# Kernel tuning notes

Hardware: AMD Instinct MI355X
Metric: run time of the kernel (lower is better)

Reference implementation:

```python
import jax, jax.numpy as jnp
import numpy as np

B, CAP, H, NH = 128, 65536, 512, 8
HD = H // NH
GH = H // 4  # gate hidden


def setup_inputs() -> dict:
    key = jax.random.key(0)
    ks = jax.random.split(key, 8)
    s = 1.0 / np.sqrt(H)
    sg = 1.0 / np.sqrt(GH)
    return {
        "query": jax.random.normal(ks[0], (B, H), jnp.float32),
        "memory_keys": jax.random.normal(ks[1], (CAP, H), jnp.float32) * s,
        "memory_values": jax.random.normal(ks[2], (CAP, H), jnp.float32) * s,
        "in_proj_w": jax.random.normal(ks[3], (3 * H, H), jnp.float32) * s,
        "in_proj_b": jnp.zeros((3 * H,), jnp.float32),
        "out_proj_w": jax.random.normal(ks[4], (H, H), jnp.float32) * s,
        "out_proj_b": jnp.zeros((H,), jnp.float32),
        "gate_w1": jax.random.normal(ks[5], (GH, H), jnp.float32) * s,
        "gate_b1": jnp.zeros((GH,), jnp.float32),
        "gate_w2": jax.random.normal(ks[6], (1, GH), jnp.float32) * sg,
        "gate_b2": jnp.zeros((1,), jnp.float32),
        "usage_count": jnp.zeros((CAP,), jnp.float32),
        "last_used": jnp.zeros((CAP,), jnp.float32),
        "step_counter": 1,
    }


def reference(query, memory_keys, memory_values, in_proj_w, in_proj_b,
              out_proj_w, out_proj_b, gate_w1, gate_b1, gate_w2, gate_b2,
              usage_count, last_used, step_counter):
    # nn.MultiheadAttention packed projections: rows [0:H]=Wq, [H:2H]=Wk, [2H:3H]=Wv
    wq, wk, wv = in_proj_w[:H], in_proj_w[H:2 * H], in_proj_w[2 * H:]
    bq, bk, bv = in_proj_b[:H], in_proj_b[H:2 * H], in_proj_b[2 * H:]

    q = (query @ wq.T + bq).reshape(B, NH, HD)           # [B, h, d] (q_len = 1)
    k = (memory_keys @ wk.T + bk).reshape(CAP, NH, HD)   # [C, h, d]
    v = (memory_values @ wv.T + bv).reshape(CAP, NH, HD)  # [C, h, d]

    scores = jnp.einsum('bhd,chd->bhc', q, k) / np.sqrt(HD)  # [B, h, C]
    attn = jax.nn.softmax(scores, axis=-1)
    ctx = jnp.einsum('bhc,chd->bhd', attn, v).reshape(B, H)
    attn_out = ctx @ out_proj_w.T + out_proj_b               # [B, H]

    # usage bookkeeping: attn_weights averaged over heads, then over batch
    avg_attn = attn.mean(axis=(0, 1))                        # [C]
    new_usage = usage_count + avg_attn
    new_last = jnp.where(avg_attn > 1e-3,
                         jnp.float32(step_counter), last_used)

    # gating MLP: Linear -> ReLU -> Linear -> Sigmoid
    gate = jax.nn.sigmoid(
        jax.nn.relu(query @ gate_w1.T + gate_b1) @ gate_w2.T + gate_b2)  # [B, 1]
    memory_output = gate * attn_out                          # [B, H]
    return memory_output, new_usage, new_last
```

## Files before the change

### kernel.cpp

```cpp
#include <hip/hip_runtime.h>
#include <stdint.h>


typedef __bf16 b16x8 __attribute__((ext_vector_type(8)));
typedef float f32x4 __attribute__((ext_vector_type(4)));

static __device__ __forceinline__ unsigned short f2bf(float f) {
  return __builtin_bit_cast(unsigned short, (__bf16)f);
}

static __device__ __forceinline__ f32x4 MFMA(b16x8 a, b16x8 b, f32x4 c) {
  return __builtin_amdgcn_mfma_f32_16x16x32_bf16(a, b, c, 0, 0, 0);
}

#define GLL16(g, l)                                                          \
  __builtin_amdgcn_global_load_lds(                                          \
      (const __attribute__((address_space(1))) void*)(g),                    \
      (__attribute__((address_space(3))) void*)(l), 16, 0, 0)

__global__ void k_convert_w(const float* __restrict__ w, unsigned short* __restrict__ dst) {
  int i = blockIdx.x * 256 + threadIdx.x;
  float4 v = reinterpret_cast<const float4*>(w + 512 * 512)[i];
  ushort4 o;
  o.x = f2bf(v.x); o.y = f2bf(v.y); o.z = f2bf(v.z); o.w = f2bf(v.w);
  reinterpret_cast<ushort4*>(dst)[i] = o;
}

__global__ void k_proj_q(const float* __restrict__ query, const float* __restrict__ w,
                         const float* __restrict__ bias, unsigned short* __restrict__ qout) {
  __shared__ float qs[512];
  int b = blockIdx.x, j = threadIdx.x;
  qs[j] = query[b * 512 + j];
  __syncthreads();
  float acc = bias[j];
  const float4* q4 = reinterpret_cast<const float4*>(qs);
  const float4* w4 = reinterpret_cast<const float4*>(w + j * 512);
#pragma unroll 8
  for (int i = 0; i < 128; ++i) {
    float4 a = q4[i], c = w4[i];
    acc += a.x * c.x + a.y * c.y + a.z * c.z + a.w * c.w;
  }
  qout[b * 512 + j] = f2bf(acc);
}

__global__ void k_gate(const float* __restrict__ query, const float* __restrict__ w1,
                       const float* __restrict__ b1, const float* __restrict__ w2,
                       const float* __restrict__ b2, float* __restrict__ gate) {
  __shared__ float qs[512];
  __shared__ float red[2];
  int b = blockIdx.x, j = threadIdx.x;
  qs[j] = query[b * 512 + j];
  qs[j + 128] = query[b * 512 + j + 128];
  qs[j + 256] = query[b * 512 + j + 256];
  qs[j + 384] = query[b * 512 + j + 384];
  __syncthreads();
  float acc = b1[j];
  const float4* q4 = reinterpret_cast<const float4*>(qs);
  const float4* w4 = reinterpret_cast<const float4*>(w1 + j * 512);
#pragma unroll 8
  for (int i = 0; i < 128; ++i) {
    float4 a = q4[i], c = w4[i];
    acc += a.x * c.x + a.y * c.y + a.z * c.z + a.w * c.w;
  }
  float t = fmaxf(acc, 0.f) * w2[j];
#pragma unroll
  for (int off = 1; off < 64; off <<= 1) t += __shfl_xor(t, off, 64);
  if ((j & 63) == 0) red[j >> 6] = t;
  __syncthreads();
  if (j == 0) {
    float z = red[0] + red[1] + b2[0];
    gate[b] = 1.f / (1.f + __builtin_amdgcn_exp2f(-z * 1.44269504088896f));
  }
}

__global__ __launch_bounds__(512, 4) void k_proj_kv(
    const float* __restrict__ mk, const float* __restrict__ mv,
    const unsigned short* __restrict__ wkb, const unsigned short* __restrict__ wvb,
    const float* __restrict__ in_b,
    unsigned short* __restrict__ kout, unsigned short* __restrict__ vtout) {
  const int p = blockIdx.x;
  const int xcd = p & 7, slot = p >> 3;
  const int isV = xcd >> 2;
  const int j0 = (slot & 3) * 128;
  const int c0 = (xcd & 3) * 16384 + (slot >> 2) * 128;
  const float* Ag = isV ? mv : mk;
  const unsigned short* W = isV ? wvb : wkb;
  const float* bias = in_b + (isV ? 1024 : 512);
  const int tid = threadIdx.x;
  const int w = tid >> 6, wr = w >> 2, wc = w & 3;
  const int ln = tid & 15, g = (tid & 63) >> 4;
  const int sw = (ln >> 1) & 3;

  __shared__ __align__(16) unsigned short Al[2][128 * 32];
  __shared__ __align__(16) unsigned short Wl[2][128 * 32];

  f32x4 acc[4][2];
#pragma unroll
  for (int m = 0; m < 4; ++m)
#pragma unroll
    for (int n = 0; n < 2; ++n) acc[m][n] = {0.f, 0.f, 0.f, 0.f};

  const int arow = tid >> 2, aq = tid & 3;
  const float* aptr = Ag + (size_t)(c0 + arow) * 512 + aq * 8;
  const int aoff = arow * 32 + ((aq ^ ((arow >> 1) & 3)) << 3);

  const int lane = tid & 63;
  const int wrow = 16 * w + (lane >> 2);
  const int wps = (lane & 3) ^ ((wrow >> 1) & 3);
  const unsigned short* wsrc = W + (size_t)(j0 + wrow) * 512 + wps * 8;
  const int wdoff = w * 512;

  float4 aA0, aA1, aB0, aB1;
  {
    GLL16(wsrc, &Wl[0][wdoff]);
    const float4* ap = reinterpret_cast<const float4*>(aptr);
    aA0 = ap[0]; aA1 = ap[1];
    b16x8 v;
    v[0] = (__bf16)aA0.x; v[1] = (__bf16)aA0.y; v[2] = (__bf16)aA0.z; v[3] = (__bf16)aA0.w;
    v[4] = (__bf16)aA1.x; v[5] = (__bf16)aA1.y; v[6] = (__bf16)aA1.z; v[7] = (__bf16)aA1.w;
    *reinterpret_cast<b16x8*>(&Al[0][aoff]) = v;
    const float4* ap1 = reinterpret_cast<const float4*>(aptr + 32);
    aB0 = ap1[0]; aB1 = ap1[1];
  }
  __syncthreads();

#pragma unroll 2
  for (int kk = 0; kk < 16; ++kk) {
    const int cur = kk & 1, nxt = cur ^ 1;
    if (kk < 14) {
      const float4* ap = reinterpret_cast<const float4*>(aptr + (kk + 2) * 32);
      if (cur == 0) { aA0 = ap[0]; aA1 = ap[1]; }
      else          { aB0 = ap[0]; aB1 = ap[1]; }
    }
    if (kk < 15) GLL16(wsrc + (kk + 1) * 32, &Wl[nxt][wdoff]);

    b16x8 af[4], wf[2];
#pragma unroll
    for (int m = 0; m < 4; ++m) {
      int row = 64 * wr + 16 * m + ln;
      af[m] = *reinterpret_cast<const b16x8*>(&Al[cur][row * 32 + ((g ^ sw) << 3)]);
    }
#pragma unroll
    for (int n = 0; n < 2; ++n) {
      int row = 32 * wc + 16 * n + ln;
      wf[n] = *reinterpret_cast<const b16x8*>(&Wl[cur][row * 32 + ((g ^ sw) << 3)]);
    }
    if (!isV) {
#pragma unroll
      for (int m = 0; m < 4; ++m)
#pragma unroll
        for (int n = 0; n < 2; ++n) acc[m][n] = MFMA(wf[n], af[m], acc[m][n]);
    } else {
#pragma unroll
      for (int m = 0; m < 4; ++m)
#pragma unroll
        for (int n = 0; n < 2; ++n) acc[m][n] = MFMA(af[m], wf[n], acc[m][n]);
    }
    if (kk < 15) {
      float4 f0 = (nxt == 0) ? aA0 : aB0, f1 = (nxt == 0) ? aA1 : aB1;
      b16x8 v;
      v[0] = (__bf16)f0.x; v[1] = (__bf16)f0.y; v[2] = (__bf16)f0.z; v[3] = (__bf16)f0.w;
      v[4] = (__bf16)f1.x; v[5] = (__bf16)f1.y; v[6] = (__bf16)f1.z; v[7] = (__bf16)f1.w;
      *reinterpret_cast<b16x8*>(&Al[nxt][aoff]) = v;
    }
    __syncthreads();
  }

  if (!isV) {
#pragma unroll
    for (int m = 0; m < 4; ++m) {
      int c = c0 + 64 * wr + 16 * m + ln;
#pragma unroll
      for (int n = 0; n < 2; ++n) {
        int jb = j0 + 32 * wc + 16 * n + 4 * g;
        float4 bb = *reinterpret_cast<const float4*>(&bias[jb]);
        ushort4 o;
        o.x = f2bf(acc[m][n][0] + bb.x);
        o.y = f2bf(acc[m][n][1] + bb.y);
        o.z = f2bf(acc[m][n][2] + bb.z);
        o.w = f2bf(acc[m][n][3] + bb.w);
        *reinterpret_cast<ushort4*>(&kout[(size_t)c * 512 + jb]) = o;
      }
    }
  } else {
#pragma unroll
    for (int n = 0; n < 2; ++n) {
      int j = j0 + 32 * wc + 16 * n + ln;
      float bj = bias[j];
#pragma unroll
      for (int m = 0; m < 4; ++m) {
        int cb = c0 + 64 * wr + 16 * m + 4 * g;
        ushort4 o;
        o.x = f2bf(acc[m][n][0] + bj);
        o.y = f2bf(acc[m][n][1] + bj);
        o.z = f2bf(acc[m][n][2] + bj);
        o.w = f2bf(acc[m][n][3] + bj);
        *reinterpret_cast<ushort4*>(&vtout[(size_t)j * 65536 + cb]) = o;
      }
    }
  }
}

__global__ __launch_bounds__(256) void k_attn1(
    const unsigned short* __restrict__ kb, const unsigned short* __restrict__ vt,
    const unsigned short* __restrict__ qb,
    float* __restrict__ l_ws, float* __restrict__ ctxT) {
  const int h = blockIdx.y, cg = blockIdx.x;
  const int tid = threadIdx.x;
  const int wv = tid >> 6, wr = wv >> 1, wc = wv & 1;
  const int ln = tid & 15, g = (tid & 63) >> 4;
  __shared__ __align__(16) unsigned short kS[128 * 64];
  __shared__ __align__(16) unsigned short pS[128 * 128];
  __shared__ __align__(16) unsigned short vS[64 * 128];
  const float SC = 0.125f * 1.44269504088896f;

  b16x8 qf[4][2];
#pragma unroll
  for (int n = 0; n < 4; ++n)
#pragma unroll
    for (int ks = 0; ks < 2; ++ks) {
      int b = 64 * wc + 16 * n + ln;
      qf[n][ks] = *reinterpret_cast<const b16x8*>(&qb[(size_t)b * 512 + h * 64 + ks * 32 + g * 8]);
    }
  f32x4 pacc[2][4];
#pragma unroll
  for (int m = 0; m < 2; ++m)
#pragma unroll
    for (int n = 0; n < 4; ++n) pacc[m][n] = {0.f, 0.f, 0.f, 0.f};
  float lsum[4] = {0.f, 0.f, 0.f, 0.f};

  for (int it = 0; it < 8; ++it) {
    int c0g = cg * 1024 + it * 128;
#pragma unroll
    for (int i = 0; i < 4; ++i) {
      int fl = i * 256 + tid, row = fl >> 3, p8 = fl & 7;
      uint4 d = *reinterpret_cast<const uint4*>(&kb[(size_t)(c0g + row) * 512 + h * 64 + p8 * 8]);
      *reinterpret_cast<uint4*>(&kS[(row * 8 + (p8 ^ (row & 7))) * 8]) = d;
    }
#pragma unroll
    for (int i = 0; i < 4; ++i) {
      int fl = i * 256 + tid, row = fl >> 4, p16 = fl & 15;
      uint4 d = *reinterpret_cast<const uint4*>(&vt[(size_t)(h * 64 + row) * 65536 + c0g + p16 * 8]);
      *reinterpret_cast<uint4*>(&vS[(row * 16 + (p16 ^ (row & 7))) * 8]) = d;
    }
    __syncthreads();

    f32x4 sacc[4][4];
#pragma unroll
    for (int m = 0; m < 4; ++m)
#pragma unroll
      for (int n = 0; n < 4; ++n) sacc[m][n] = {0.f, 0.f, 0.f, 0.f};
#pragma unroll
    for (int ks = 0; ks < 2; ++ks) {
      b16x8 a[4];
#pragma unroll
      for (int m = 0; m < 4; ++m) {
        int row = 64 * wr + 16 * m + ln;
        a[m] = *reinterpret_cast<const b16x8*>(&kS[(row * 8 + ((ks * 4 + g) ^ (row & 7))) * 8]);
      }
#pragma unroll
      for (int m = 0; m < 4; ++m)
#pragma unroll
        for (int n = 0; n < 4; ++n) sacc[m][n] = MFMA(a[m], qf[n][ks], sacc[m][n]);
    }
#pragma unroll
    for (int m = 0; m < 4; ++m)
#pragma unroll
      for (int n = 0; n < 4; ++n) {
        float p0 = __builtin_amdgcn_exp2f(sacc[m][n][0] * SC);
        float p1 = __builtin_amdgcn_exp2f(sacc[m][n][1] * SC);
        float p2 = __builtin_amdgcn_exp2f(sacc[m][n][2] * SC);
        float p3 = __builtin_amdgcn_exp2f(sacc[m][n][3] * SC);
        lsum[n] += (p0 + p1) + (p2 + p3);
        int b = 64 * wc + 16 * n + ln;
        int c = 64 * wr + 16 * m + 4 * g;
        int base = b * 128 + (((c >> 3) ^ (b & 7)) * 8) + (c & 7);
        ushort2 lo, hi;
        lo.x = f2bf(p0); lo.y = f2bf(p1);
        hi.x = f2bf(p2); hi.y = f2bf(p3);
        *reinterpret_cast<ushort2*>(&pS[base]) = lo;
        *reinterpret_cast<ushort2*>(&pS[base + 2]) = hi;
      }
    __syncthreads();
#pragma unroll
    for (int ks = 0; ks < 4; ++ks) {
      b16x8 av[2], bp[4];
#pragma unroll
      for (int m = 0; m < 2; ++m) {
        int row = 32 * wr + 16 * m + ln;
        av[m] = *reinterpret_cast<const b16x8*>(&vS[(row * 16 + ((ks * 4 + g) ^ (row & 7))) * 8]);
      }
#pragma unroll
      for (int n = 0; n < 4; ++n) {
        int row = 64 * wc + 16 * n + ln;
        bp[n] = *reinterpret_cast<const b16x8*>(&pS[(row * 16 + ((ks * 4 + g) ^ (row & 7))) * 8]);
      }
#pragma unroll
      for (int m = 0; m < 2; ++m)
#pragma unroll
        for (int n = 0; n < 4; ++n) pacc[m][n] = MFMA(av[m], bp[n], pacc[m][n]);
    }
    __syncthreads();
  }
#pragma unroll
  for (int n = 0; n < 4; ++n) {
    float v = lsum[n];
    v += __shfl_xor(v, 16, 64);
    v += __shfl_xor(v, 32, 64);
    if ((tid & 63) < 16) atomicAdd(&l_ws[h * 128 + 64 * wc + 16 * n + ln], v);
  }
#pragma unroll
  for (int m = 0; m < 2; ++m)
#pragma unroll
    for (int n = 0; n < 4; ++n)
#pragma unroll
      for (int r = 0; r < 4; ++r) {
        int d = 32 * wr + 16 * m + 4 * g + r;
        int b = 64 * wc + 16 * n + ln;
        atomicAdd(&ctxT[(h * 64 + d) * 128 + b], pacc[m][n][r]);
      }
}

__global__ __launch_bounds__(256) void k_attn2(
    const unsigned short* __restrict__ kb, const unsigned short* __restrict__ qb,
    const float* __restrict__ l_ws, float* __restrict__ avgA) {
  const int h = blockIdx.y, cg = blockIdx.x;
  const int tid = threadIdx.x;
  const int wv = tid >> 6, wr = wv >> 1, wc = wv & 1;
  const int ln = tid & 15, g = (tid & 63) >> 4;
  __shared__ __align__(16) unsigned short kS[128 * 64];
  __shared__ float wS[128];
  const float SC = 0.125f * 1.44269504088896f;
  if (tid < 128) wS[tid] = 1.f / l_ws[h * 128 + tid];
  b16x8 qf[4][2];
#pragma unroll
  for (int n = 0; n < 4; ++n)
#pragma unroll
    for (int ks = 0; ks < 2; ++ks) {
      int b = 64 * wc + 16 * n + ln;
      qf[n][ks] = *reinterpret_cast<const b16x8*>(&qb[(size_t)b * 512 + h * 64 + ks * 32 + g * 8]);
    }
  __syncthreads();
  float wn[4];
#pragma unroll
  for (int n = 0; n < 4; ++n) wn[n] = wS[64 * wc + 16 * n + ln];

  for (int it = 0; it < 8; ++it) {
    int c0g = cg * 1024 + it * 128;
#pragma unroll
    for (int i = 0; i < 4; ++i) {
      int fl = i * 256 + tid, row = fl >> 3, p8 = fl & 7;
      uint4 d = *reinterpret_cast<const uint4*>(&kb[(size_t)(c0g + row) * 512 + h * 64 + p8 * 8]);
      *reinterpret_cast<uint4*>(&kS[(row * 8 + (p8 ^ (row & 7))) * 8]) = d;
    }
    __syncthreads();
    f32x4 sacc[4][4];
#pragma unroll
    for (int m = 0; m < 4; ++m)
#pragma unroll
      for (int n = 0; n < 4; ++n) sacc[m][n] = {0.f, 0.f, 0.f, 0.f};
#pragma unroll
    for (int ks = 0; ks < 2; ++ks) {
      b16x8 a[4];
#pragma unroll
      for (int m = 0; m < 4; ++m) {
        int row = 64 * wr + 16 * m + ln;
        a[m] = *reinterpret_cast<const b16x8*>(&kS[(row * 8 + ((ks * 4 + g) ^ (row & 7))) * 8]);
      }
#pragma unroll
      for (int m = 0; m < 4; ++m)
#pragma unroll
        for (int n = 0; n < 4; ++n) sacc[m][n] = MFMA(a[m], qf[n][ks], sacc[m][n]);
    }
#pragma unroll
    for (int m = 0; m < 4; ++m) {
      float s0 = 0.f, s1 = 0.f, s2 = 0.f, s3 = 0.f;
#pragma unroll
      for (int n = 0; n < 4; ++n) {
        s0 += __builtin_amdgcn_exp2f(sacc[m][n][0] * SC) * wn[n];
        s1 += __builtin_amdgcn_exp2f(sacc[m][n][1] * SC) * wn[n];
        s2 += __builtin_amdgcn_exp2f(sacc[m][n][2] * SC) * wn[n];
        s3 += __builtin_amdgcn_exp2f(sacc[m][n][3] * SC) * wn[n];
      }
#pragma unroll
      for (int off = 1; off < 16; off <<= 1) {
        s0 += __shfl_xor(s0, off, 64);
        s1 += __shfl_xor(s1, off, 64);
        s2 += __shfl_xor(s2, off, 64);
        s3 += __shfl_xor(s3, off, 64);
      }
      if (ln == 0) {
        int c = c0g + 64 * wr + 16 * m + 4 * g;
        atomicAdd(&avgA[c], s0);
        atomicAdd(&avgA[c + 1], s1);
        atomicAdd(&avgA[c + 2], s2);
        atomicAdd(&avgA[c + 3], s3);
      }
    }
    __syncthreads();
  }
}

__global__ void k_finalize(const float* __restrict__ ctxT, const float* __restrict__ l_ws,
                           const float* __restrict__ wout, const float* __restrict__ bout,
                           const float* __restrict__ gate, float* __restrict__ out) {
  __shared__ float cs[512];
  int b = blockIdx.x, j = threadIdx.x;
  cs[j] = ctxT[j * 128 + b] / l_ws[(j >> 6) * 128 + b];
  __syncthreads();
  float acc = bout[j];
  const float4* c4 = reinterpret_cast<const float4*>(cs);
  const float4* w4 = reinterpret_cast<const float4*>(wout + j * 512);
#pragma unroll 8
  for (int i = 0; i < 128; ++i) {
    float4 a = c4[i], c = w4[i];
    acc += a.x * c.x + a.y * c.y + a.z * c.z + a.w * c.w;
  }
  out[b * 512 + j] = gate[b] * acc;
}

__global__ void k_usage(const float* __restrict__ avgA, const float* __restrict__ usage,
                        const float* __restrict__ last, const int* __restrict__ step,
                        float* __restrict__ out_usage, float* __restrict__ out_last) {
  int c = blockIdx.x * 256 + threadIdx.x;
  float avg = avgA[c] * (1.f / 1024.f);
  out_usage[c] = usage[c] + avg;
  out_last[c] = (avg > 0.001f) ? (float)step[0] : last[c];
}

extern "C" void kernel_launch(void* const* d_in, const int* in_sizes, int n_in,
                              void* d_out, int out_size, void* d_ws, size_t ws_size,
                              hipStream_t stream) {
  const float* query = (const float*)d_in[0];
  const float* mk    = (const float*)d_in[1];
  const float* mv    = (const float*)d_in[2];
  const float* in_w  = (const float*)d_in[3];
  const float* in_b  = (const float*)d_in[4];
  const float* out_w = (const float*)d_in[5];
  const float* out_b = (const float*)d_in[6];
  const float* gw1   = (const float*)d_in[7];
  const float* gb1   = (const float*)d_in[8];
  const float* gw2   = (const float*)d_in[9];
  const float* gb2   = (const float*)d_in[10];
  const float* usage = (const float*)d_in[11];
  const float* last  = (const float*)d_in[12];
  const int*   step  = (const int*)d_in[13];

  char* ws = (char*)d_ws;
  unsigned short* qb  = (unsigned short*)(ws);
  unsigned short* wkb = (unsigned short*)(ws + 131072);
  unsigned short* wvb = (unsigned short*)(ws + 655360);
  unsigned short* kb  = (unsigned short*)(ws + 1179648);
  unsigned short* vt  = (unsigned short*)(ws + 68288512);
  float* l_ws = (float*)(ws + 135397376);
  float* ctxT = (float*)(ws + 135401472);
  float* avgA = (float*)(ws + 135663616);
  float* gate = (float*)(ws + 135925760);
  float* out = (float*)d_out;

  hipMemsetAsync(ws + 135397376, 0, 4096 + 262144 + 262144, stream);

  k_convert_w<<<512, 256, 0, stream>>>(in_w, wkb);
  k_proj_q<<<128, 512, 0, stream>>>(query, in_w, in_b, qb);
  k_gate<<<128, 128, 0, stream>>>(query, gw1, gb1, gw2, gb2, gate);
  k_proj_kv<<<4096, 512, 0, stream>>>(mk, mv, wkb, wvb, in_b, kb, vt);
  k_attn1<<<dim3(64, 8), 256, 0, stream>>>(kb, vt, qb, l_ws, ctxT);
  k_attn2<<<dim3(64, 8), 256, 0, stream>>>(kb, qb, l_ws, avgA);
  k_finalize<<<128, 512, 0, stream>>>(ctxT, l_ws, out_w, out_b, gate, out);
  k_usage<<<256, 256, 0, stream>>>(avgA, usage, last, step, out + 65536, out + 131072);
}
```

Baseline: 371.7 us.

## Stage full 128-row A tile in LDS once and loop over all output column tiles

The K/V projection kernel now converts a whole 128x512 block of memory keys/values to bf16 into LDS once (128 KB, XOR-swizzled), then iterates over all four 128-column output tiles. Each fp32 input row is read from global memory once instead of four times. Weight tiles stream through a 4-slot LDS ring via global_load_lds, with explicit vmcnt waits and sched barriers in place of full __syncthreads. The grid shrinks to 1024 blocks and launch bounds drop to 2 blocks per CU, trading occupancy and load/compute overlap during the A staging phase for less global traffic.

After: 345.7 us. 1.08x faster.

```diff
diff --git a/kernel.cpp b/kernel.cpp
--- a/kernel.cpp
+++ b/kernel.cpp
@@ -17,6 +17,8 @@
   __builtin_amdgcn_global_load_lds(                                          \
       (const __attribute__((address_space(1))) void*)(g),                    \
       (__attribute__((address_space(3))) void*)(l), 16, 0, 0)
+
+#define SBAR() __builtin_amdgcn_sched_barrier(0)
 
 __global__ void k_convert_w(const float* __restrict__ w, unsigned short* __restrict__ dst) {
   int i = blockIdx.x * 256 + threadIdx.x;
@@ -73,132 +75,127 @@
   }
 }
 
-__global__ __launch_bounds__(512, 4) void k_proj_kv(
+__global__ __launch_bounds__(512, 2) void k_proj_kv(
     const float* __restrict__ mk, const float* __restrict__ mv,
     const unsigned short* __restrict__ wkb, const unsigned short* __restrict__ wvb,
     const float* __restrict__ in_b,
     unsigned short* __restrict__ kout, unsigned short* __restrict__ vtout) {
   const int p = blockIdx.x;
-  const int xcd = p & 7, slot = p >> 3;
-  const int isV = xcd >> 2;
-  const int j0 = (slot & 3) * 128;
-  const int c0 = (xcd & 3) * 16384 + (slot >> 2) * 128;
+  const int isV = p & 1;
+  const int c0 = (p >> 1) * 128;
   const float* Ag = isV ? mv : mk;
   const unsigned short* W = isV ? wvb : wkb;
   const float* bias = in_b + (isV ? 1024 : 512);
   const int tid = threadIdx.x;
-  const int w = tid >> 6, wr = w >> 2, wc = w & 3;
+  const int w = tid >> 6, lane = tid & 63;
+  const int wr = w >> 2, wc = w & 3;
   const int ln = tid & 15, g = (tid & 63) >> 4;
-  const int sw = (ln >> 1) & 3;
-
-  __shared__ __align__(16) unsigned short Al[2][128 * 32];
-  __shared__ __align__(16) unsigned short Wl[2][128 * 32];
-
-  f32x4 acc[4][2];
-#pragma unroll
-  for (int m = 0; m < 4; ++m)
-#pragma unroll
-    for (int n = 0; n < 2; ++n) acc[m][n] = {0.f, 0.f, 0.f, 0.f};
-
-  const int arow = tid >> 2, aq = tid & 3;
-  const float* aptr = Ag + (size_t)(c0 + arow) * 512 + aq * 8;
-  const int aoff = arow * 32 + ((aq ^ ((arow >> 1) & 3)) << 3);
-
-  const int lane = tid & 63;
+
+  __shared__ __align__(16) unsigned short AL[65536];
+  __shared__ __align__(16) unsigned short WL[4][4096];
+
   const int wrow = 16 * w + (lane >> 2);
-  const int wps = (lane & 3) ^ ((wrow >> 1) & 3);
-  const unsigned short* wsrc = W + (size_t)(j0 + wrow) * 512 + wps * 8;
-  const int wdoff = w * 512;
-
-  float4 aA0, aA1, aB0, aB1;
-  {
-    GLL16(wsrc, &Wl[0][wdoff]);
-    const float4* ap = reinterpret_cast<const float4*>(aptr);
-    aA0 = ap[0]; aA1 = ap[1];
+  const int wcs = (lane & 3) ^ ((wrow >> 1) & 3);
+  const unsigned short* wsrc = W + (size_t)wrow * 512 + wcs * 8;
+  const int wdst = w * 512;
+
+  GLL16(wsrc, &WL[0][wdst]);
+  GLL16(wsrc + 32, &WL[1][wdst]);
+
+#pragma unroll 4
+  for (int c = 0; c < 16; ++c) {
+    int row = c * 8 + w;
+    const float* src = Ag + (size_t)(c0 + row) * 512 + lane * 8;
+    float4 f0 = *reinterpret_cast<const float4*>(src);
+    float4 f1 = *reinterpret_cast<const float4*>(src + 4);
     b16x8 v;
-    v[0] = (__bf16)aA0.x; v[1] = (__bf16)aA0.y; v[2] = (__bf16)aA0.z; v[3] = (__bf16)aA0.w;
-    v[4] = (__bf16)aA1.x; v[5] = (__bf16)aA1.y; v[6] = (__bf16)aA1.z; v[7] = (__bf16)aA1.w;
-    *reinterpret_cast<b16x8*>(&Al[0][aoff]) = v;
-    const float4* ap1 = reinterpret_cast<const float4*>(aptr + 32);
-    aB0 = ap1[0]; aB1 = ap1[1];
-  }
-  __syncthreads();
-
-#pragma unroll 2
-  for (int kk = 0; kk < 16; ++kk) {
-    const int cur = kk & 1, nxt = cur ^ 1;
-    if (kk < 14) {
-      const float4* ap = reinterpret_cast<const float4*>(aptr + (kk + 2) * 32);
-      if (cur == 0) { aA0 = ap[0]; aA1 = ap[1]; }
-      else          { aB0 = ap[0]; aB1 = ap[1]; }
-    }
-    if (kk < 15) GLL16(wsrc + (kk + 1) * 32, &Wl[nxt][wdoff]);
-
-    b16x8 af[4], wf[2];
-#pragma unroll
-    for (int m = 0; m < 4; ++m) {
-      int row = 64 * wr + 16 * m + ln;
-      af[m] = *reinterpret_cast<const b16x8*>(&Al[cur][row * 32 + ((g ^ sw) << 3)]);
-    }
-#pragma unroll
-    for (int n = 0; n < 2; ++n) {
-      int row = 32 * wc + 16 * n + ln;
-      wf[n] = *reinterpret_cast<const b16x8*>(&Wl[cur][row * 32 + ((g ^ sw) << 3)]);
-    }
+    v[0] = (__bf16)f0.x; v[1] = (__bf16)f0.y; v[2] = (__bf16)f0.z; v[3] = (__bf16)f0.w;
+    v[4] = (__bf16)f1.x; v[5] = (__bf16)f1.y; v[6] = (__bf16)f1.z; v[7] = (__bf16)f1.w;
+    int chunk = lane ^ (row & 7);
+    *reinterpret_cast<b16x8*>(&AL[row * 512 + chunk * 8]) = v;
+  }
+  __syncthreads();
+
+#pragma unroll
+  for (int jt = 0; jt < 4; ++jt) {
+    const int j0 = jt * 128;
+    f32x4 acc[4][2];
+#pragma unroll
+    for (int m = 0; m < 4; ++m)
+#pragma unroll
+      for (int n = 0; n < 2; ++n) acc[m][n] = {0.f, 0.f, 0.f, 0.f};
+
+#pragma unroll
+    for (int kk = 0; kk < 16; ++kk) {
+      const int t = jt * 16 + kk;
+      const int tn = (t + 2 <= 63) ? t + 2 : 63;
+      const int slot = (t + 2) & 3;
+      GLL16(wsrc + (size_t)(tn >> 4) * 65536 + (tn & 15) * 32, &WL[slot][wdst]);
+      SBAR();
+      asm volatile("s_waitcnt vmcnt(2)" ::: "memory");
+      SBAR();
+      __builtin_amdgcn_s_barrier();
+      SBAR();
+      b16x8 af[4], wf[2];
+#pragma unroll
+      for (int m = 0; m < 4; ++m) {
+        int r = 64 * wr + 16 * m + ln;
+        int ch = (kk * 4 + g) ^ (r & 7);
+        af[m] = *reinterpret_cast<const b16x8*>(&AL[r * 512 + ch * 8]);
+      }
+#pragma unroll
+      for (int n = 0; n < 2; ++n) {
+        int r = 32 * wc + 16 * n + ln;
+        wf[n] = *reinterpret_cast<const b16x8*>(&WL[t & 3][r * 32 + ((g ^ ((r >> 1) & 3)) << 3)]);
+      }
+      if (!isV) {
+#pragma unroll
+        for (int m = 0; m < 4; ++m)
+#pragma unroll
+          for (int n = 0; n < 2; ++n) acc[m][n] = MFMA(wf[n], af[m], acc[m][n]);
+      } else {
+#pragma unroll
+        for (int m = 0; m < 4; ++m)
+#pragma unroll
+          for (int n = 0; n < 2; ++n) acc[m][n] = MFMA(af[m], wf[n], acc[m][n]);
+      }
+    }
+
     if (!isV) {
 #pragma unroll
-      for (int m = 0; m < 4; ++m)
-#pragma unroll
-        for (int n = 0; n < 2; ++n) acc[m][n] = MFMA(wf[n], af[m], acc[m][n]);
+      for (int m = 0; m < 4; ++m) {
+        int c = c0 + 64 * wr + 16 * m + ln;
+#pragma unroll
+        for (int n = 0; n < 2; ++n) {
+          int jb = j0 + 32 * wc + 16 * n + 4 * g;
+          float4 bb = *reinterpret_cast<const float4*>(&bias[jb]);
+          ushort4 o;
+          o.x = f2bf(acc[m][n][0] + bb.x);
+          o.y = f2bf(acc[m][n][1] + bb.y);
+          o.z = f2bf(acc[m][n][2] + bb.z);
+          o.w = f2bf(acc[m][n][3] + bb.w);
+          *reinterpret_cast<ushort4*>(&kout[(size_t)c * 512 + jb]) = o;
+        }
+      }
     } else {
 #pragma unroll
-      for (int m = 0; m < 4; ++m)
-#pragma unroll
-        for (int n = 0; n < 2; ++n) acc[m][n] = MFMA(af[m], wf[n], acc[m][n]);
-    }
-    if (kk < 15) {
-      float4 f0 = (nxt == 0) ? aA0 : aB0, f1 = (nxt == 0) ? aA1 : aB1;
-      b16x8 v;
-      v[0] = (__bf16)f0.x; v[1] = (__bf16)f0.y; v[2] = (__bf16)f0.z; v[3] = (__bf16)f0.w;
-      v[4] = (__bf16)f1.x; v[5] = (__bf16)f1.y; v[6] = (__bf16)f1.z; v[7] = (__bf16)f1.w;
-      *reinterpret_cast<b16x8*>(&Al[nxt][aoff]) = v;
-    }
-    __syncthreads();
-  }
-
-  if (!isV) {
-#pragma unroll
-    for (int m = 0; m < 4; ++m) {
-      int c = c0 + 64 * wr + 16 * m + ln;
-#pragma unroll
       for (int n = 0; n < 2; ++n) {
-        int jb = j0 + 32 * wc + 16 * n + 4 * g;
-        float4 bb = *reinterpret_cast<const float4*>(&bias[jb]);
-        ushort4 o;
-        o.x = f2bf(acc[m][n][0] + bb.x);
-        o.y = f2bf(acc[m][n][1] + bb.y);
-        o.z = f2bf(acc[m][n][2] + bb.z);
-        o.w = f2bf(acc[m][n][3] + bb.w);
-        *reinterpret_cast<ushort4*>(&kout[(size_t)c * 512 + jb]) = o;
-      }
-    }
-  } else {
-#pragma unroll
-    for (int n = 0; n < 2; ++n) {
-      int j = j0 + 32 * wc + 16 * n + ln;
-      float bj = bias[j];
-#pragma unroll
-      for (int m = 0; m < 4; ++m) {
-        int cb = c0 + 64 * wr + 16 * m + 4 * g;
-        ushort4 o;
-        o.x = f2bf(acc[m][n][0] + bj);
-        o.y = f2bf(acc[m][n][1] + bj);
-        o.z = f2bf(acc[m][n][2] + bj);
-        o.w = f2bf(acc[m][n][3] + bj);
-        *reinterpret_cast<ushort4*>(&vtout[(size_t)j * 65536 + cb]) = o;
-      }
-    }
-  }
+        int j = j0 + 32 * wc + 16 * n + ln;
+        float bj = bias[j];
+#pragma unroll
+        for (int m = 0; m < 4; ++m) {
+          int cb = c0 + 64 * wr + 16 * m + 4 * g;
+          ushort4 o;
+          o.x = f2bf(acc[m][n][0] + bj);
+          o.y = f2bf(acc[m][n][1] + bj);
+          o.z = f2bf(acc[m][n][2] + bj);
+          o.w = f2bf(acc[m][n][3] + bj);
+          *reinterpret_cast<ushort4*>(&vtout[(size_t)j * 65536 + cb]) = o;
+        }
+      }
+    }
+  }
+  asm volatile("s_waitcnt vmcnt(0)" ::: "memory");
 }
 
 __global__ __launch_bounds__(256) void k_attn1(
@@ -463,7 +460,7 @@
   k_convert_w<<<512, 256, 0, stream>>>(in_w, wkb);
   k_proj_q<<<128, 512, 0, stream>>>(query, in_w, in_b, qb);
   k_gate<<<128, 128, 0, stream>>>(query, gw1, gb1, gw2, gb2, gate);
-  k_proj_kv<<<4096, 512, 0, stream>>>(mk, mv, wkb, wvb, in_b, kb, vt);
+  k_proj_kv<<<1024, 512, 0, stream>>>(mk, mv, wkb, wvb, in_b, kb, vt);
   k_attn1<<<dim3(64, 8), 256, 0, stream>>>(kb, vt, qb, l_ws, ctxT);
   k_attn2<<<dim3(64, 8), 256, 0, stream>>>(kb, qb, l_ws, avgA);
   k_finalize<<<128, 512, 0, stream>>>(ctxT, l_ws, out_w, out_b, gate, out);
```
